# Kernel tuning notes

Measured on AMD Instinct MI355X. Metric: run time of the kernel, lower is better.

Reference implementation:

```python
import jax, jax.numpy as jnp
import numpy as np


def setup_inputs() -> dict:
    key = jax.random.key(0)
    k1, k2, k3 = jax.random.split(key, 3)
    B, C, H, W = 64, 256, 32, 32   # batch, hidden_dim, latent grid
    D, K = 128, 1024               # latent_dim, num_embeddings
    z = jax.random.normal(k1, (B, C, H, W), dtype=jnp.float32)
    proj_w = jax.random.normal(k2, (D, C), dtype=jnp.float32) * 0.02  # 1x1 conv kernel [out,in]
    proj_b = jnp.zeros((D,), jnp.float32)
    # codebook init uniform(-1/K, 1/K) as in torch module
    embed = (jax.random.uniform(k3, (K, D), dtype=jnp.float32) * 2.0 - 1.0) / K
    return {"z": z, "proj_w": proj_w, "proj_b": proj_b, "embed": embed}


def reference(z, proj_w, proj_b, embed):
    # 1x1 conv projection: [B,C,H,W] -> [B,H,W,D]  (fuses conv + permute)
    zp = jnp.einsum('bchw,dc->bhwd', z, proj_w) + proj_b
    B, H, W, D = zp.shape
    zf = zp.reshape(-1, D)                                   # [N, D], N = B*H*W
    # squared Euclidean distance to codebook: ||z||^2 - 2 z.e + ||e||^2  -> [N, K]
    dist = (jnp.sum(zf * zf, axis=1, keepdims=True)
            - 2.0 * (zf @ embed.T)
            + jnp.sum(embed * embed, axis=1))
    min_indices = jnp.argmin(dist, axis=1)                   # [N]
    z_q = embed[min_indices].reshape(B, H, W, D)             # codebook gather
    # straight-through estimator
    rep_z_q = zp + jax.lax.stop_gradient(z_q - zp)
    rep_z_q = rep_z_q.transpose(0, 3, 1, 2)                  # back to NCHW
    return rep_z_q, min_indices
```

## Files before the change

### kernel.cpp

```cpp
#include <hip/hip_runtime.h>

#define B_   64
#define C_   256
#define D_   128
#define HW_  1024
#define K_   1024
#define N_   65536
#define MARGIN_PREF 1.2e-3f

typedef __attribute__((ext_vector_type(8))) short short8;
typedef __attribute__((ext_vector_type(4))) float f32x4;

__device__ __forceinline__ unsigned short f2bf(float f) {
    unsigned u = __float_as_uint(f);
    return (unsigned short)((u + 0x7FFFu + ((u >> 16) & 1u)) >> 16);
}
__device__ __forceinline__ unsigned long long packdk(float d, int k) {
    unsigned u = __float_as_uint(d);
    u = (u & 0x80000000u) ? ~u : (u | 0x80000000u);
    return ((unsigned long long)u << 10) | (unsigned)k;
}
__device__ __forceinline__ float unpackd(unsigned long long key) {
    unsigned u = (unsigned)(key >> 10);
    u = (u & 0x80000000u) ? (u ^ 0x80000000u) : ~u;
    return __uint_as_float(u);
}
__device__ __forceinline__ unsigned long long min64(unsigned long long a, unsigned long long b) {
    return a < b ? a : b;
}

template <typename F>
__device__ __forceinline__ float np_sum128(F ld) {
#pragma clang fp contract(off)
    float r0 = ld(0), r1 = ld(1), r2 = ld(2), r3 = ld(3);
    float r4 = ld(4), r5 = ld(5), r6 = ld(6), r7 = ld(7);
#pragma unroll
    for (int i = 8; i < 128; i += 8) {
        r0 = r0 + ld(i + 0); r1 = r1 + ld(i + 1);
        r2 = r2 + ld(i + 2); r3 = r3 + ld(i + 3);
        r4 = r4 + ld(i + 4); r5 = r5 + ld(i + 5);
        r6 = r6 + ld(i + 6); r7 = r7 + ld(i + 7);
    }
    return ((r0 + r1) + (r2 + r3)) + ((r4 + r5) + (r6 + r7));
}

__global__ __launch_bounds__(256) void k0_norms(const float* __restrict__ embed,
                                                float* __restrict__ enorm,
                                                unsigned short* __restrict__ ebf) {
#pragma clang fp contract(off)
    int k = blockIdx.x * 256 + threadIdx.x;
    if (k >= K_) return;
    const float* e = embed + (size_t)k * D_;
    enorm[k] = np_sum128([&](int i) { float v = e[i]; return v * v; });
    const int sw = (k & 7) << 4;
    char* rowp = (char*)ebf + ((size_t)k << 8);
#pragma unroll
    for (int j = 0; j < 16; ++j) {
        short8 v;
#pragma unroll
        for (int q = 0; q < 8; ++q) v[q] = (short)f2bf(e[j * 8 + q]);
        *(short8*)(rowp + ((j * 16) ^ sw)) = v;
    }
}

__global__ __launch_bounds__(256) void k1_proj(const float* __restrict__ z,
                                               const float* __restrict__ w,
                                               const float* __restrict__ bias,
                                               float* __restrict__ zp,
                                               unsigned short* __restrict__ zbf) {
#pragma clang fp contract(off)
    __shared__ float zs[64][64];
    __shared__ float wsh[64][128];
    const int b   = blockIdx.x >> 4;
    const int hw0 = (blockIdx.x & 15) << 6;
    const int t   = threadIdx.x;
    const int hwg = (t & 7) * 8;
    const int dg  = (t >> 3) * 4;

    float acc[8][4];
#pragma unroll
    for (int i = 0; i < 8; ++i)
#pragma unroll
        for (int j = 0; j < 4; ++j) acc[i][j] = 0.f;

    for (int ct = 0; ct < C_; ct += 64) {
        __syncthreads();
#pragma unroll
        for (int i = 0; i < 16; ++i) {
            int idx = i * 256 + t;
            int cc = idx >> 6, hwl = idx & 63;
            zs[cc][hwl] = z[(((size_t)b * C_ + ct + cc) << 10) + hw0 + hwl];
        }
#pragma unroll
        for (int i = 0; i < 32; ++i) {
            int idx = i * 256 + t;
            int cc = idx >> 7, d = idx & 127;
            wsh[cc][d] = w[(size_t)d * C_ + ct + cc];
        }
        __syncthreads();
#pragma unroll 2
        for (int cc = 0; cc < 64; ++cc) {
            float4 za = *(const float4*)&zs[cc][hwg];
            float4 zb = *(const float4*)&zs[cc][hwg + 4];
            float4 wv = *(const float4*)&wsh[cc][dg];
            float zv[8]  = {za.x, za.y, za.z, za.w, zb.x, zb.y, zb.z, zb.w};
            float wva[4] = {wv.x, wv.y, wv.z, wv.w};
#pragma unroll
            for (int i = 0; i < 8; ++i)
#pragma unroll
                for (int j = 0; j < 4; ++j) {
                    float p = zv[i] * wva[j];
                    acc[i][j] = acc[i][j] + p;
                }
        }
    }
#pragma unroll
    for (int i = 0; i < 8; ++i)
#pragma unroll
        for (int j = 0; j < 4; ++j) {
            float v = acc[i][j] + bias[dg + j];
            size_t off = (((size_t)b * HW_ + hw0 + hwg + i) << 7) + dg + j;
            zp[off]  = v;
            zbf[off] = f2bf(v);
        }
}

__global__ __launch_bounds__(256) void k0z_znorm(const float* __restrict__ zp,
                                                 float* __restrict__ znorm) {
#pragma clang fp contract(off)
    __shared__ float zl[64][129];
    const int t = threadIdx.x, n0 = blockIdx.x * 64;
#pragma unroll
    for (int i = 0; i < 32; ++i) {
        int idx = i * 256 + t;
        zl[idx >> 7][idx & 127] = zp[(size_t)n0 * 128 + idx];
    }
    __syncthreads();
    if (t < 64)
        znorm[n0 + t] = np_sum128([&](int i) { float v = zl[t][i]; return v * v; });
}

__global__ __launch_bounds__(256) void k2_argmin(const unsigned short* __restrict__ zbf,
                                                 const unsigned short* __restrict__ ebf,
                                                 const float* __restrict__ zp,
                                                 const float* __restrict__ embed,
                                                 const float* __restrict__ enorm,
                                                 const float* __restrict__ znorm,
                                                 int* __restrict__ bestk_ws,
                                                 float* __restrict__ out_idx) {
    __shared__ unsigned char etile[2][64 * 256];
    __shared__ float els[1024];
    const int t   = threadIdx.x;
    const int l   = t & 63;
    const int wid = t >> 6;
    const int r0  = blockIdx.x * 128 + wid * 32;
    const int lr  = l & 15;
    const int lh  = l >> 4;

    short8 zfrag[2][4];
#pragma unroll
    for (int rt = 0; rt < 2; ++rt)
#pragma unroll
        for (int dt = 0; dt < 4; ++dt)
            zfrag[rt][dt] = *(const short8*)(zbf + (((size_t)(r0 + rt * 16 + lr)) << 7) + dt * 32 + lh * 8);

    const int swz = (lr & 7) << 4;
    int roff[4];
#pragma unroll
    for (int dt = 0; dt < 4; ++dt)
        roff[dt] = lr * 256 + ((dt * 64 + lh * 16) ^ swz);

    const char* ebf_b = (const char*)ebf;
    auto STAGE = [&](int st, int b) {
#pragma unroll
        for (int j = 0; j < 4; ++j) {
            int off = j * 4096 + (t << 4);
            __builtin_amdgcn_global_load_lds(
                (const __attribute__((address_space(1))) void*)(ebf_b + ((size_t)st << 14) + off),
                (__attribute__((address_space(3))) void*)(&etile[b][off]),
                16, 0, 0);
        }
    };

#pragma unroll
    for (int i = 0; i < 4; ++i) els[i * 256 + t] = enorm[i * 256 + t];

    float bmin0 = 1e30f, bmin1 = 1e30f;
    STAGE(0, 0);
#pragma unroll 1
    for (int st = 0; st < 16; ++st) {
        __syncthreads();
        if (st < 15) STAGE(st + 1, (st + 1) & 1);
        const unsigned char* buf = etile[st & 1];
#pragma unroll
        for (int kf = 0; kf < 4; ++kf) {
            short8 af[4];
#pragma unroll
            for (int dt = 0; dt < 4; ++dt)
                af[dt] = *(const short8*)(buf + kf * 4096 + roff[dt]);
            f32x4 en4 = *(const f32x4*)(els + st * 64 + kf * 16 + lh * 4);
            f32x4 a0 = {0.f, 0.f, 0.f, 0.f};
            f32x4 a1 = {0.f, 0.f, 0.f, 0.f};
#pragma unroll
            for (int dt = 0; dt < 4; ++dt)
                a0 = __builtin_amdgcn_mfma_f32_16x16x32_bf16(af[dt], zfrag[0][dt], a0, 0, 0, 0);
#pragma unroll
            for (int dt = 0; dt < 4; ++dt)
                a1 = __builtin_amdgcn_mfma_f32_16x16x32_bf16(af[dt], zfrag[1][dt], a1, 0, 0, 0);
#pragma unroll
            for (int reg = 0; reg < 4; ++reg) {
                bmin0 = fminf(bmin0, fmaf(-2.f, a0[reg], en4[reg]));
                bmin1 = fminf(bmin1, fmaf(-2.f, a1[reg], en4[reg]));
            }
        }
    }
    {
        bmin0 = fminf(bmin0, __shfl_xor(bmin0, 16, 64));
        bmin0 = fminf(bmin0, __shfl_xor(bmin0, 32, 64));
        bmin1 = fminf(bmin1, __shfl_xor(bmin1, 16, 64));
        bmin1 = fminf(bmin1, __shfl_xor(bmin1, 32, 64));
    }
    const float thr0 = bmin0 + MARGIN_PREF;
    const float thr1 = bmin1 + MARGIN_PREF;

    unsigned long long ca0 = 0, cb0 = 0, ca1 = 0, cb1 = 0;
    int cnt0 = 0, cnt1 = 0;
    __syncthreads();
    STAGE(0, 0);
#pragma unroll 1
    for (int st = 0; st < 16; ++st) {
        __syncthreads();
        if (st < 15) STAGE(st + 1, (st + 1) & 1);
        const unsigned char* buf = etile[st & 1];
#pragma unroll
        for (int kf = 0; kf < 4; ++kf) {
            short8 af[4];
#pragma unroll
            for (int dt = 0; dt < 4; ++dt)
                af[dt] = *(const short8*)(buf + kf * 4096 + roff[dt]);
            f32x4 en4 = *(const f32x4*)(els + st * 64 + kf * 16 + lh * 4);
            f32x4 a0 = {0.f, 0.f, 0.f, 0.f};
            f32x4 a1 = {0.f, 0.f, 0.f, 0.f};
#pragma unroll
            for (int dt = 0; dt < 4; ++dt)
                a0 = __builtin_amdgcn_mfma_f32_16x16x32_bf16(af[dt], zfrag[0][dt], a0, 0, 0, 0);
#pragma unroll
            for (int dt = 0; dt < 4; ++dt)
                a1 = __builtin_amdgcn_mfma_f32_16x16x32_bf16(af[dt], zfrag[1][dt], a1, 0, 0, 0);
#pragma unroll
            for (int reg = 0; reg < 4; ++reg) {
                int kk = st * 64 + kf * 16 + lh * 4 + reg;
                float d0 = fmaf(-2.f, a0[reg], en4[reg]);
                if (d0 < thr0) {
                    if (cnt0 < 6)       ca0 |= (unsigned long long)kk << (10 * cnt0);
                    else if (cnt0 < 12) cb0 |= (unsigned long long)kk << (10 * (cnt0 - 6));
                    ++cnt0;
                }
                float d1 = fmaf(-2.f, a1[reg], en4[reg]);
                if (d1 < thr1) {
                    if (cnt1 < 6)       ca1 |= (unsigned long long)kk << (10 * cnt1);
                    else if (cnt1 < 12) cb1 |= (unsigned long long)kk << (10 * (cnt1 - 6));
                    ++cnt1;
                }
            }
        }
    }

    unsigned long long fin[2];
#pragma unroll
    for (int rt = 0; rt < 2; ++rt) {
        const int myrow = r0 + rt * 16 + lr;
        const float* zrow = zp + ((size_t)myrow << 7);
        const float  zn   = znorm[myrow];
        unsigned long long best = ~0ull;
        unsigned long long ca = rt == 0 ? ca0 : ca1, cb = rt == 0 ? cb0 : cb1;
        int cnt = rt == 0 ? cnt0 : cnt1;

        auto refine = [&](int kk) {
#pragma clang fp contract(off)
            const float* e = embed + ((size_t)kk << 7);
            float s = 0.f;
#pragma unroll 1
            for (int d = 0; d < 128; ++d) s = fmaf(zrow[d], e[d], s);
            float T  = 2.0f * s;
            float A  = zn - T;
            float Bv = A + enorm[kk];
            best = min64(best, packdk(Bv, kk));
        };

        if (cnt <= 12) {
#pragma unroll
            for (int i = 0; i < 6; ++i)
                if (i < cnt) refine((int)((ca >> (10 * i)) & 1023ull));
#pragma unroll
            for (int i = 6; i < 12; ++i)
                if (i < cnt) refine((int)((cb >> (10 * (i - 6))) & 1023ull));
        } else {
#pragma unroll 1
            for (int st = 0; st < 16; ++st)
#pragma unroll
                for (int kf = 0; kf < 4; ++kf)
#pragma unroll
                    for (int reg = 0; reg < 4; ++reg)
                        refine(st * 64 + kf * 16 + lh * 4 + reg);
        }
        unsigned long long o;
        o = __shfl_xor(best, 16, 64); best = min64(best, o);
        o = __shfl_xor(best, 32, 64); best = min64(best, o);
        fin[rt] = best;
    }

    if (l < 16) {
#pragma unroll
        for (int rt = 0; rt < 2; ++rt) {
            int row = r0 + rt * 16 + l;
            int kk  = (int)(fin[rt] & 1023ull);
            bestk_ws[row] = kk;
            out_idx[row]  = (float)kk;
        }
    }
}

__global__ __launch_bounds__(256) void k3_gather(const float* __restrict__ embed,
                                                 const int* __restrict__ bestk,
                                                 float* __restrict__ out0) {
    __shared__ float tile[64][129];
    const int b   = blockIdx.x >> 4;
    const int hw0 = (blockIdx.x & 15) << 6;
    const int t   = threadIdx.x;
    const int n0  = b * HW_ + hw0;
#pragma unroll
    for (int i = 0; i < 32; ++i) {
        int idx = i * 256 + t;
        int hwl = idx >> 7, d = idx & 127;
        int k = bestk[n0 + hwl];
        tile[hwl][d] = embed[(size_t)k * 128 + d];
    }
    __syncthreads();
#pragma unroll
    for (int i = 0; i < 32; ++i) {
        int idx = i * 256 + t;
        int d = idx >> 6, hwl = idx & 63;
        out0[(((size_t)b * D_ + d) << 10) + hw0 + hwl] = tile[hwl][d];
    }
}

extern "C" void kernel_launch(void* const* d_in, const int* in_sizes, int n_in,
                              void* d_out, int out_size, void* d_ws, size_t ws_size,
                              hipStream_t stream) {
    const float* z     = (const float*)d_in[0];
    const float* pw    = (const float*)d_in[1];
    const float* pb    = (const float*)d_in[2];
    const float* embed = (const float*)d_in[3];

    float* out0 = (float*)d_out;
    float* out1 = (float*)d_out + (size_t)B_ * D_ * HW_;

    char* ws = (char*)d_ws;
    float*          zp    = (float*)ws;
    unsigned short* zbf   = (unsigned short*)(ws + (32u << 20));
    unsigned short* ebf   = (unsigned short*)(ws + (48u << 20));
    float*          enorm = (float*)(ws + (48u << 20) + (256u << 10));
    float*          znorm = (float*)(ws + (49u << 20));
    int*            bestk = (int*)  (ws + (50u << 20));

    hipLaunchKernelGGL(k0_norms,  dim3(4),    dim3(256), 0, stream, embed, enorm, ebf);
    hipLaunchKernelGGL(k1_proj,   dim3(1024), dim3(256), 0, stream, z, pw, pb, zp, zbf);
    hipLaunchKernelGGL(k0z_znorm, dim3(1024), dim3(256), 0, stream, zp, znorm);
    hipLaunchKernelGGL(k2_argmin, dim3(512),  dim3(256), 0, stream,
                       zbf, ebf, zp, embed, enorm, znorm, bestk, out1);
    hipLaunchKernelGGL(k3_gather, dim3(1024), dim3(256), 0, stream, embed, bestk, out0);
}
```

Baseline: 369.5 us.

## Fuse z-norm into projection kernel and codebook gather into argmin kernel

The row-norm computation moves into the projection kernel, which stages its output tile in shared memory and sums squares there, so the separate znorm kernel no longer re-reads zp from global memory. The codebook gather and NCHW transpose move into the argmin kernel, which keeps the winning indices in shared memory instead of writing and re-reading a bestk workspace. Together these drop two kernel launches and their global round trips. The cost is more shared memory and extra barriers in the fused kernels, plus a serialized gather tail at the end of the argmin blocks.

```diff
diff --git a/kernel.cpp b/kernel.cpp
--- a/kernel.cpp
+++ b/kernel.cpp
@@ -19,11 +19,6 @@
     unsigned u = __float_as_uint(d);
     u = (u & 0x80000000u) ? ~u : (u | 0x80000000u);
     return ((unsigned long long)u << 10) | (unsigned)k;
-}
-__device__ __forceinline__ float unpackd(unsigned long long key) {
-    unsigned u = (unsigned)(key >> 10);
-    u = (u & 0x80000000u) ? (u ^ 0x80000000u) : ~u;
-    return __uint_as_float(u);
 }
 __device__ __forceinline__ unsigned long long min64(unsigned long long a, unsigned long long b) {
     return a < b ? a : b;
@@ -67,10 +62,12 @@
                                                const float* __restrict__ w,
                                                const float* __restrict__ bias,
                                                float* __restrict__ zp,
-                                               unsigned short* __restrict__ zbf) {
+                                               unsigned short* __restrict__ zbf,
+                                               float* __restrict__ znorm) {
 #pragma clang fp contract(off)
-    __shared__ float zs[64][64];
-    __shared__ float wsh[64][128];
+    __shared__ float smem1[64 * 64 + 64 * 128];
+    float (*zs)[64]   = (float(*)[64])smem1;
+    float (*wsh)[128] = (float(*)[128])(smem1 + 4096);
     const int b   = blockIdx.x >> 4;
     const int hw0 = (blockIdx.x & 15) << 6;
     const int t   = threadIdx.x;
@@ -114,6 +111,7 @@
                 }
         }
     }
+    float vv[8][4];
 #pragma unroll
     for (int i = 0; i < 8; ++i)
 #pragma unroll
@@ -122,22 +120,20 @@
             size_t off = (((size_t)b * HW_ + hw0 + hwg + i) << 7) + dg + j;
             zp[off]  = v;
             zbf[off] = f2bf(v);
-        }
-}
-
-__global__ __launch_bounds__(256) void k0z_znorm(const float* __restrict__ zp,
-                                                 float* __restrict__ znorm) {
-#pragma clang fp contract(off)
-    __shared__ float zl[64][129];
-    const int t = threadIdx.x, n0 = blockIdx.x * 64;
-#pragma unroll
-    for (int i = 0; i < 32; ++i) {
-        int idx = i * 256 + t;
-        zl[idx >> 7][idx & 127] = zp[(size_t)n0 * 128 + idx];
-    }
+            vv[i][j] = v;
+        }
+
+    __syncthreads();
+    float (*ztile)[129] = (float(*)[129])smem1;
+#pragma unroll
+    for (int i = 0; i < 8; ++i)
+#pragma unroll
+        for (int j = 0; j < 4; ++j)
+            ztile[hwg + i][dg + j] = vv[i][j];
     __syncthreads();
     if (t < 64)
-        znorm[n0 + t] = np_sum128([&](int i) { float v = zl[t][i]; return v * v; });
+        znorm[(size_t)b * HW_ + hw0 + t] =
+            np_sum128([&](int i) { float v2 = ztile[t][i]; return v2 * v2; });
 }
 
 __global__ __launch_bounds__(256) void k2_argmin(const unsigned short* __restrict__ zbf,
@@ -146,14 +142,17 @@
                                                  const float* __restrict__ embed,
                                                  const float* __restrict__ enorm,
                                                  const float* __restrict__ znorm,
-                                                 int* __restrict__ bestk_ws,
+                                                 float* __restrict__ out0,
                                                  float* __restrict__ out_idx) {
-    __shared__ unsigned char etile[2][64 * 256];
-    __shared__ float els[1024];
+    __shared__ __align__(16) char smem[36864];
+    __shared__ int kks[128];
+    unsigned char (*etile)[16384] = (unsigned char(*)[16384])smem;
+    float* els = (float*)(smem + 32768);
     const int t   = threadIdx.x;
     const int l   = t & 63;
     const int wid = t >> 6;
-    const int r0  = blockIdx.x * 128 + wid * 32;
+    const int rb  = blockIdx.x * 128;
+    const int r0  = rb + wid * 32;
     const int lr  = l & 15;
     const int lh  = l >> 4;
 
@@ -313,35 +312,32 @@
     if (l < 16) {
 #pragma unroll
         for (int rt = 0; rt < 2; ++rt) {
-            int row = r0 + rt * 16 + l;
-            int kk  = (int)(fin[rt] & 1023ull);
-            bestk_ws[row] = kk;
-            out_idx[row]  = (float)kk;
-        }
-    }
-}
-
-__global__ __launch_bounds__(256) void k3_gather(const float* __restrict__ embed,
-                                                 const int* __restrict__ bestk,
-                                                 float* __restrict__ out0) {
-    __shared__ float tile[64][129];
-    const int b   = blockIdx.x >> 4;
-    const int hw0 = (blockIdx.x & 15) << 6;
-    const int t   = threadIdx.x;
-    const int n0  = b * HW_ + hw0;
-#pragma unroll
-    for (int i = 0; i < 32; ++i) {
-        int idx = i * 256 + t;
-        int hwl = idx >> 7, d = idx & 127;
-        int k = bestk[n0 + hwl];
-        tile[hwl][d] = embed[(size_t)k * 128 + d];
+            int kk = (int)(fin[rt] & 1023ull);
+            kks[wid * 32 + rt * 16 + l] = kk;
+            out_idx[r0 + rt * 16 + l]   = (float)kk;
+        }
     }
     __syncthreads();
-#pragma unroll
-    for (int i = 0; i < 32; ++i) {
-        int idx = i * 256 + t;
-        int d = idx >> 6, hwl = idx & 63;
-        out0[(((size_t)b * D_ + d) << 10) + hw0 + hwl] = tile[hwl][d];
+
+    float (*gtile)[132] = (float(*)[132])smem;
+    const int bb  = rb >> 10;
+    const int hw0 = rb & 1023;
+#pragma unroll 1
+    for (int sub = 0; sub < 2; ++sub) {
+#pragma unroll
+        for (int i = 0; i < 32; ++i) {
+            int idx = i * 256 + t;
+            int hwl = idx >> 7, d = idx & 127;
+            gtile[hwl][d] = embed[(size_t)kks[sub * 64 + hwl] * 128 + d];
+        }
+        __syncthreads();
+#pragma unroll
+        for (int i = 0; i < 32; ++i) {
+            int idx = i * 256 + t;
+            int d = idx >> 6, hwl = idx & 63;
+            out0[(((size_t)bb * D_ + d) << 10) + hw0 + sub * 64 + hwl] = gtile[hwl][d];
+        }
+        __syncthreads();
     }
 }
 
@@ -362,12 +358,9 @@
     unsigned short* ebf   = (unsigned short*)(ws + (48u << 20));
     float*          enorm = (float*)(ws + (48u << 20) + (256u << 10));
     float*          znorm = (float*)(ws + (49u << 20));
-    int*            bestk = (int*)  (ws + (50u << 20));
 
     hipLaunchKernelGGL(k0_norms,  dim3(4),    dim3(256), 0, stream, embed, enorm, ebf);
-    hipLaunchKernelGGL(k1_proj,   dim3(1024), dim3(256), 0, stream, z, pw, pb, zp, zbf);
-    hipLaunchKernelGGL(k0z_znorm, dim3(1024), dim3(256), 0, stream, zp, znorm);
+    hipLaunchKernelGGL(k1_proj,   dim3(1024), dim3(256), 0, stream, z, pw, pb, zp, zbf, znorm);
     hipLaunchKernelGGL(k2_argmin, dim3(512),  dim3(256), 0, stream,
-                       zbf, ebf, zp, embed, enorm, znorm, bestk, out1);
-    hipLaunchKernelGGL(k3_gather, dim3(1024), dim3(256), 0, stream, embed, bestk, out0);
-}
+                       zbf, ebf, zp, embed, enorm, znorm, out0, out1);
+}
```

New measurement: 478.0 us. 29.4% more time.
